# Performance work log

Measured on AMD Instinct MI355X. Metric: run time of the kernel, lower is better.

The kernel has to match this reference:

```python
import jax, jax.numpy as jnp
import numpy as np

B, S, D, H, M = 4, 4096, 768, 12, 256
Dh = D // H
EPS_KERNEL = 1e-4
LN_EPS = 1e-5


def setup_inputs() -> dict:
    key = jax.random.key(0)
    ks = jax.random.split(key, 18)
    w = lambda k, sh: jax.random.normal(k, sh, jnp.float32) * 0.02
    return {
        "x": jax.random.normal(ks[0], (B, S, D), jnp.float32),
        # FAVOR+ random projection (performer uses orthogonal gaussian; gaussian here, same math)
        "proj": jax.random.normal(ks[1], (M, Dh), jnp.float32),
        "wq": w(ks[2], (D, D)), "bq": jnp.zeros((D,), jnp.float32),
        "wk": w(ks[3], (D, D)), "bk": jnp.zeros((D,), jnp.float32),
        "wv": w(ks[4], (D, D)), "bv": jnp.zeros((D,), jnp.float32),
        "wo": w(ks[5], (D, D)), "bo": jnp.zeros((D,), jnp.float32),
        "ln1_g": jnp.ones((D,), jnp.float32), "ln1_b": jnp.zeros((D,), jnp.float32),
        "ln2_g": jnp.ones((D,), jnp.float32), "ln2_b": jnp.zeros((D,), jnp.float32),
        "w1": w(ks[6], (4 * D, D)), "b1": jnp.zeros((4 * D,), jnp.float32),
        "w2": w(ks[7], (D, 4 * D)), "b2": jnp.zeros((D,), jnp.float32),
    }


def layernorm(x, g, b):
    mu = x.mean(-1, keepdims=True)
    var = ((x - mu) ** 2).mean(-1, keepdims=True)
    return (x - mu) / jnp.sqrt(var + LN_EPS) * g + b


def softmax_features(data, proj, is_query):
    # FAVOR+ positive softmax kernel features (performer-pytorch softmax_kernel)
    norm = data.shape[-1] ** -0.25
    ratio = proj.shape[0] ** -0.5
    dd = jnp.einsum('bhnd,md->bhnm', data * norm, proj)       # [B,H,S,M]
    diag = (data ** 2).sum(-1, keepdims=True) * 0.5 * norm * norm
    if is_query:
        mx = jnp.max(dd, axis=-1, keepdims=True)
    else:
        mx = jnp.max(dd)
    return ratio * (jnp.exp(dd - diag - mx) + EPS_KERNEL)


def performer_block(x, proj, wq, bq, wk, bk, wv, bv, wo, bo,
                    ln1_g, ln1_b, ln2_g, ln2_b, w1, b1, w2, b2):
    h = layernorm(x, ln1_g, ln1_b)
    split = lambda t: t.reshape(B, S, H, Dh).transpose(0, 2, 1, 3)  # [B,H,S,Dh]
    q = split(h @ wq.T + bq)
    k = split(h @ wk.T + bk)
    v = split(h @ wv.T + bv)

    qp = softmax_features(q, proj, True)    # [B,H,S,M]
    kp = softmax_features(k, proj, False)   # [B,H,S,M]

    # non-causal linear attention
    k_sum = kp.sum(axis=2)                                   # [B,H,M]
    d_inv = 1.0 / jnp.einsum('bhnm,bhm->bhn', qp, k_sum)     # [B,H,S]
    ctx = jnp.einsum('bhnm,bhnd->bhmd', kp, v)               # [B,H,M,Dh]
    attn = jnp.einsum('bhnm,bhmd,bhn->bhnd', qp, ctx, d_inv) # [B,H,S,Dh]
    attn = attn.transpose(0, 2, 1, 3).reshape(B, S, D)
    x = x + attn @ wo.T + bo

    h2 = layernorm(x, ln2_g, ln2_b)
    h2 = jax.nn.gelu(h2 @ w1.T + b1, approximate=False)
    x = x + h2 @ w2.T + b2
    return x


def reference(x, proj, wq, bq, wk, bk, wv, bv, wo, bo,
              ln1_g, ln1_b, ln2_g, ln2_b, w1, b1, w2, b2):
    return performer_block(x, proj, wq, bq, wk, bk, wv, bv, wo, bo,
                           ln1_g, ln1_b, ln2_g, ln2_b, w1, b1, w2, b2)
```

## Files before the change

kernel.cpp:

```cpp
#include <hip/hip_runtime.h>
#include <math.h>

typedef __attribute__((ext_vector_type(8))) short bf16x8;
typedef __attribute__((ext_vector_type(4))) float f32x4;

__device__ __forceinline__ float b2f(unsigned short u) {
    return __uint_as_float(((unsigned)u) << 16);
}
__device__ __forceinline__ unsigned short f2b(float f) {
    unsigned u = __float_as_uint(f);
    u += 0x7FFF + ((u >> 16) & 1);
    return (unsigned short)(u >> 16);
}
__device__ __forceinline__ void up2(unsigned u, float& a, float& b) {
    a = __uint_as_float(u << 16);
    b = __uint_as_float(u & 0xffff0000u);
}
__device__ __forceinline__ float gelu_exact(float v) {
    return 0.5f * v * (1.0f + erff(v * 0.70710678118654752f));
}
__device__ __forceinline__ void atomicMaxFloat(float* addr, float val) {
    unsigned* ua = (unsigned*)addr;
    unsigned old = *ua;
    while (true) {
        float of = __uint_as_float(old);
        if (of >= val) break;
        unsigned assumed = old;
        old = atomicCAS(ua, assumed, __float_as_uint(val));
        if (old == assumed) break;
    }
}
__device__ __forceinline__ void gl_lds16(const unsigned short* g, unsigned short* lds) {
    __builtin_amdgcn_global_load_lds((const __attribute__((address_space(1))) unsigned int*)g,
                                     (__attribute__((address_space(3))) unsigned int*)lds, 16, 0, 0);
}

__global__ void init_kernel(float* ksum, float* kmax) {
    int i = blockIdx.x * 256 + threadIdx.x;
    if (i < 48 * 256) ksum[i] = 0.0f;
    if (i == 0) *kmax = -3.0e38f;
}

__global__ __launch_bounds__(256)
void cvt_qkvp(const float* __restrict__ wq, const float* __restrict__ wk, const float* __restrict__ wv,
              const float* __restrict__ prj, unsigned short* __restrict__ wdst,
              unsigned short* __restrict__ pdst) {
    int i4 = (blockIdx.x * 256 + threadIdx.x) * 4;
    const float* s; unsigned short* d; int off;
    if (i4 < 1769472) { s = (i4 < 589824) ? wq : (i4 < 1179648 ? wk : wv);
        off = (i4 < 589824) ? i4 : (i4 < 1179648 ? i4 - 589824 : i4 - 1179648);
        d = wdst + i4; }
    else { s = prj; off = i4 - 1769472; d = pdst + off; }
    float4 v = *(const float4*)&s[off];
    ushort4 o; o.x = f2b(v.x); o.y = f2b(v.y); o.z = f2b(v.z); o.w = f2b(v.w);
    *(ushort4*)d = o;
}
__global__ __launch_bounds__(256)
void cvt_ow12(const float* __restrict__ wo, const float* __restrict__ w1, const float* __restrict__ w2,
              unsigned short* __restrict__ dst) {
    int i4 = (blockIdx.x * 256 + threadIdx.x) * 4;
    const float* s; int off;
    if (i4 < 589824) { s = wo; off = i4; }
    else if (i4 < 2949120) { s = w1; off = i4 - 589824; }
    else { s = w2; off = i4 - 2949120; }
    float4 v = *(const float4*)&s[off];
    ushort4 o; o.x = f2b(v.x); o.y = f2b(v.y); o.z = f2b(v.z); o.w = f2b(v.w);
    *(ushort4*)&dst[i4] = o;
}

template <bool IN_F32>
__global__ __launch_bounds__(256)
void ln_kernel(const void* __restrict__ Xv, const float* __restrict__ G,
               const float* __restrict__ Bb, unsigned short* __restrict__ OUT) {
    int row = blockIdx.x, t = threadIdx.x, wave = t >> 6, lane = t & 63;
    __shared__ float red[4];
    float x0, x1, x2;
    if constexpr (IN_F32) {
        const float* xr = (const float*)Xv + (size_t)row * 768;
        x0 = xr[t]; x1 = xr[t + 256]; x2 = xr[t + 512];
    } else {
        const unsigned short* xr = (const unsigned short*)Xv + (size_t)row * 768;
        x0 = b2f(xr[t]); x1 = b2f(xr[t + 256]); x2 = b2f(xr[t + 512]);
    }
    float s = x0 + x1 + x2;
#pragma unroll
    for (int d = 32; d; d >>= 1) s += __shfl_xor(s, d, 64);
    if (lane == 0) red[wave] = s;
    __syncthreads();
    float mean = (red[0] + red[1] + red[2] + red[3]) * (1.0f / 768.0f);
    __syncthreads();
    float d0 = x0 - mean, d1 = x1 - mean, d2 = x2 - mean;
    float s2 = d0 * d0 + d1 * d1 + d2 * d2;
#pragma unroll
    for (int d = 32; d; d >>= 1) s2 += __shfl_xor(s2, d, 64);
    if (lane == 0) red[wave] = s2;
    __syncthreads();
    float var = (red[0] + red[1] + red[2] + red[3]) * (1.0f / 768.0f);
    float inv = rsqrtf(var + 1e-5f);
    size_t base = (size_t)row * 768;
    OUT[base + t]       = f2b(d0 * inv * G[t]       + Bb[t]);
    OUT[base + t + 256] = f2b(d1 * inv * G[t + 256] + Bb[t + 256]);
    OUT[base + t + 512] = f2b(d2 * inv * G[t + 512] + Bb[t + 512]);
}

template <int EPI, bool R_F32, bool C_F32>
__global__ __launch_bounds__(512)
void gemm_bt_256(const unsigned short* __restrict__ A, const unsigned short* __restrict__ Bm,
                 const float* __restrict__ bias, const void* __restrict__ R,
                 void* __restrict__ C, int N, int K, float alpha) {
    __shared__ unsigned short sA[2][256 * 32];
    __shared__ unsigned short sB[2][128 * 32];
    const int t = threadIdx.x;
    const int wave = t >> 6, lane = t & 63, quad = lane >> 4, l16 = lane & 15;
    const int nwg = gridDim.x * gridDim.y;
    int flat = blockIdx.y * gridDim.x + blockIdx.x;
    int q = nwg >> 3, r = nwg & 7;
    int xcd = flat & 7, idx = flat >> 3;
    int swz = (xcd < r ? xcd * (q + 1) : r * (q + 1) + (xcd - r) * q) + idx;
    const int m0 = (swz / gridDim.x) * 256;
    const int n0 = (swz % gridDim.x) * 128;
    const int wm = (wave >> 1) * 64, wn = (wave & 1) * 64;
    const int srow = t >> 2;
    const int scol = ((t & 3) ^ (srow & 3)) << 3;
    const unsigned short* ga0 = &A[(size_t)(m0 + srow) * K + scol];
    const unsigned short* ga1 = &A[(size_t)(m0 + 128 + srow) * K + scol];
    const unsigned short* gb  = &Bm[(size_t)(n0 + srow) * K + scol];
    const int ldsoff = wave * 512;
    const int sw = ((quad ^ l16) & 3) << 3;
    int raoff[4], rboff[4];
#pragma unroll
    for (int i = 0; i < 4; ++i) {
        raoff[i] = (wm + i * 16 + l16) * 32 + sw;
        rboff[i] = (wn + i * 16 + l16) * 32 + sw;
    }
    f32x4 acc[4][4] = {};
    const int nt = K >> 5;
    gl_lds16(ga0, &sA[0][ldsoff]);
    gl_lds16(ga1, &sA[0][4096 + ldsoff]);
    gl_lds16(gb,  &sB[0][ldsoff]);
    __syncthreads();
    int cur = 0;
    for (int it = 0; it < nt; ++it) {
        if (it + 1 < nt) {
            const int kt = (it + 1) << 5;
            gl_lds16(ga0 + kt, &sA[cur ^ 1][ldsoff]);
            gl_lds16(ga1 + kt, &sA[cur ^ 1][4096 + ldsoff]);
            gl_lds16(gb + kt,  &sB[cur ^ 1][ldsoff]);
        }
        bf16x8 af[4], bfr[4];
#pragma unroll
        for (int i = 0; i < 4; ++i) af[i] = *(const bf16x8*)&sA[cur][raoff[i]];
#pragma unroll
        for (int j = 0; j < 4; ++j) bfr[j] = *(const bf16x8*)&sB[cur][rboff[j]];
#pragma unroll
        for (int i = 0; i < 4; ++i)
#pragma unroll
            for (int j = 0; j < 4; ++j)
                acc[i][j] = __builtin_amdgcn_mfma_f32_16x16x32_bf16(af[i], bfr[j], acc[i][j], 0, 0, 0);
        __syncthreads();
        cur ^= 1;
    }
    if constexpr (EPI == 3) {
#pragma unroll
        for (int i = 0; i < 4; ++i) {
            int rowb = m0 + wm + i * 16 + quad * 4;
            int b_ = rowb >> 12, sbase = rowb & 4095;
#pragma unroll
            for (int j = 0; j < 4; ++j) {
                int col = n0 + wn + j * 16 + l16;
                float bs = bias[col];
                ushort4 o;
                o.x = f2b(acc[i][j][0] + bs);
                o.y = f2b(acc[i][j][1] + bs);
                o.z = f2b(acc[i][j][2] + bs);
                o.w = f2b(acc[i][j][3] + bs);
                size_t dst = (((size_t)b_ * 12 + (col >> 6)) * 64 + (col & 63)) * 4096 + sbase;
                *(ushort4*)&((unsigned short*)C)[dst] = o;
            }
        }
        return;
    }
#pragma unroll
    for (int i = 0; i < 4; ++i) {
        int rowb = m0 + wm + i * 16 + quad * 4;
#pragma unroll
        for (int j = 0; j < 4; ++j) {
            int col = n0 + wn + j * 16 + l16;
            float bs = bias[col];
#pragma unroll
            for (int r4 = 0; r4 < 4; ++r4) {
                size_t idx = (size_t)(rowb + r4) * N + col;
                float v = acc[i][j][r4] + bs;
                if constexpr (EPI == 0) v *= alpha;
                if constexpr (EPI == 1) {
                    if constexpr (R_F32) v += ((const float*)R)[idx];
                    else                 v += b2f(((const unsigned short*)R)[idx]);
                }
                if constexpr (EPI == 2) v = gelu_exact(v);
                if constexpr (C_F32) ((float*)C)[idx] = v;
                else                 ((unsigned short*)C)[idx] = f2b(v);
            }
        }
    }
}

template <int MODE>
__global__ __launch_bounds__(256)
void feat_kernel(const unsigned short* __restrict__ Q, const unsigned short* __restrict__ P,
                 unsigned short* __restrict__ OUTP, float* __restrict__ kmaxp,
                 float* __restrict__ ksump) {
    __shared__ unsigned short sQ[64 * 64];
    __shared__ unsigned short sP[256 * 64];
    __shared__ float sDiag[64];
    __shared__ float sRed[4];
    int t = threadIdx.x, wave = t >> 6, lane = t & 63, quad = lane >> 4, l16 = lane & 15;
    int bh = blockIdx.y, bq = bh / 12, hh = bh % 12;
    int s0 = blockIdx.x * 64;
    size_t rowbase = (size_t)bq * 4096 + s0;
#pragma unroll
    for (int u = 0; u < 2; ++u) {
        int L = u * 256 + t, row = L >> 3, c8 = (L & 7) * 8;
        *(uint4*)&sQ[row * 64 + c8] = *(const uint4*)&Q[(rowbase + row) * 768 + hh * 64 + c8];
    }
#pragma unroll
    for (int u = 0; u < 8; ++u) {
        int L = u * 256 + t, row = L >> 3, c8 = (L & 7) * 8;
        *(uint4*)&sP[row * 64 + c8] = *(const uint4*)&P[(size_t)row * 64 + c8];
    }
    __syncthreads();
    if (MODE != 1 && t < 64) {
        float d = 0.0f;
        for (int c = 0; c < 64; ++c) { float f = b2f(sQ[t * 64 + c]); d += f * f; }
        sDiag[t] = 0.5f * d;
    }
    f32x4 acc[4][4] = {};
#pragma unroll
    for (int ks = 0; ks < 2; ++ks) {
        bf16x8 af[4], bfr[4];
#pragma unroll
        for (int i = 0; i < 4; ++i) af[i] = *(const bf16x8*)&sQ[(i * 16 + l16) * 64 + ks * 32 + quad * 8];
#pragma unroll
        for (int j = 0; j < 4; ++j) bfr[j] = *(const bf16x8*)&sP[(wave * 64 + j * 16 + l16) * 64 + ks * 32 + quad * 8];
#pragma unroll
        for (int i = 0; i < 4; ++i)
#pragma unroll
            for (int j = 0; j < 4; ++j)
                acc[i][j] = __builtin_amdgcn_mfma_f32_16x16x32_bf16(af[i], bfr[j], acc[i][j], 0, 0, 0);
    }
    if constexpr (MODE == 1) {
        float m = -3.0e38f;
#pragma unroll
        for (int i = 0; i < 4; ++i)
#pragma unroll
            for (int j = 0; j < 4; ++j)
#pragma unroll
                for (int r = 0; r < 4; ++r) m = fmaxf(m, acc[i][j][r]);
#pragma unroll
        for (int d = 1; d < 64; d <<= 1) m = fmaxf(m, __shfl_xor(m, d, 64));
        if (lane == 0) sRed[wave] = m;
        __syncthreads();
        if (t == 0) atomicMaxFloat(kmaxp, fmaxf(fmaxf(sRed[0], sRed[1]), fmaxf(sRed[2], sRed[3])));
        return;
    } else {
        __syncthreads();
        float mx_k = *kmaxp;
        float csum[4] = {0.0f, 0.0f, 0.0f, 0.0f};
#pragma unroll
        for (int i = 0; i < 4; ++i)
#pragma unroll
            for (int j = 0; j < 4; ++j) {
                int col = wave * 64 + j * 16 + l16;
                ushort4 o;
#pragma unroll
                for (int r = 0; r < 4; ++r) {
                    int row = i * 16 + quad * 4 + r;
                    float v = 0.0625f * (expf(acc[i][j][r] - sDiag[row] - mx_k) + 1e-4f);
                    csum[j] += v;
                    (&o.x)[r] = f2b(v);
                }
                *(ushort4*)&OUTP[((size_t)bh * 256 + col) * 4096 + s0 + i * 16 + quad * 4] = o;
            }
#pragma unroll
        for (int j = 0; j < 4; ++j) {
            csum[j] += __shfl_xor(csum[j], 16, 64);
            csum[j] += __shfl_xor(csum[j], 32, 64);
        }
        if (quad == 0)
#pragma unroll
            for (int j = 0; j < 4; ++j)
                atomicAdd(&ksump[bh * 256 + wave * 64 + j * 16 + l16], csum[j]);
    }
}

__global__ __launch_bounds__(256)
void ctx_gemm(const unsigned short* __restrict__ KPT, const unsigned short* __restrict__ VT,
              float* __restrict__ part) {
    __shared__ unsigned short sV[2][64 * 32];
    __shared__ unsigned short sK[2][128 * 32];
    const int t = threadIdx.x;
    const int wave = t >> 6, lane = t & 63, quad = lane >> 4, l16 = lane & 15;
    const int bh = blockIdx.y;
    const int sc = blockIdx.x >> 1, mh = blockIdx.x & 1;
    const int m0 = mh * 128;
    const int k0 = sc * 512;
    const int srow = t >> 2;
    const int scol = ((t & 3) ^ (srow & 3)) << 3;
    const unsigned short* gv  = &VT [((size_t)bh * 64 + srow) * 4096 + k0 + scol];
    const unsigned short* gk0 = &KPT[((size_t)bh * 256 + m0 + srow) * 4096 + k0 + scol];
    const unsigned short* gk1 = &KPT[((size_t)bh * 256 + m0 + 64 + srow) * 4096 + k0 + scol];
    const int ldsoff = wave * 512;
    const int sw = ((quad ^ l16) & 3) << 3;
    f32x4 acc[4][2] = {};
    gl_lds16(gv,  &sV[0][ldsoff]);
    gl_lds16(gk0, &sK[0][ldsoff]);
    gl_lds16(gk1, &sK[0][2048 + ldsoff]);
    __syncthreads();
    int cur = 0;
    for (int it = 0; it < 16; ++it) {
        if (it + 1 < 16) {
            const int kt = (it + 1) << 5;
            gl_lds16(gv + kt,  &sV[cur ^ 1][ldsoff]);
            gl_lds16(gk0 + kt, &sK[cur ^ 1][ldsoff]);
            gl_lds16(gk1 + kt, &sK[cur ^ 1][2048 + ldsoff]);
        }
        bf16x8 af[4], bfr[2];
#pragma unroll
        for (int i = 0; i < 4; ++i) af[i] = *(const bf16x8*)&sV[cur][(i * 16 + l16) * 32 + sw];
#pragma unroll
        for (int j = 0; j < 2; ++j) bfr[j] = *(const bf16x8*)&sK[cur][(wave * 32 + j * 16 + l16) * 32 + sw];
#pragma unroll
        for (int i = 0; i < 4; ++i)
#pragma unroll
            for (int j = 0; j < 2; ++j)
                acc[i][j] = __builtin_amdgcn_mfma_f32_16x16x32_bf16(af[i], bfr[j], acc[i][j], 0, 0, 0);
        __syncthreads();
        cur ^= 1;
    }
    float* base = part + ((size_t)(sc * 48 + bh) * 64) * 256;
#pragma unroll
    for (int i = 0; i < 4; ++i)
#pragma unroll
        for (int r = 0; r < 4; ++r) {
            int d = i * 16 + quad * 4 + r;
#pragma unroll
            for (int j = 0; j < 2; ++j) {
                int m = m0 + wave * 32 + j * 16 + l16;
                base[(size_t)d * 256 + m] = acc[i][j][r];
            }
        }
}

__global__ __launch_bounds__(256)
void ctx_reduce(const float* __restrict__ part, unsigned short* __restrict__ ctxb) {
    size_t i = (size_t)blockIdx.x * 256 + threadIdx.x;
    float s = 0.0f;
#pragma unroll
    for (int c = 0; c < 8; ++c) s += part[(size_t)c * 786432 + i];
    ctxb[i] = f2b(s);
}

__global__ __launch_bounds__(256)
void feat_attn(const unsigned short* __restrict__ Q, const unsigned short* __restrict__ P,
               const unsigned short* __restrict__ CTX, const float* __restrict__ ksump,
               unsigned short* __restrict__ ATT) {
    __shared__ unsigned short sQ[64 * 64];
    __shared__ unsigned short sPQ[256 * 64];
    __shared__ unsigned short sCtx[64 * 256];
    __shared__ float sDiag[64];
    __shared__ float sRed[256];
    __shared__ float sWred[256];
    __shared__ float sKs[256];
    __shared__ float sDinv[64];
    int t = threadIdx.x, wave = t >> 6, lane = t & 63, quad = lane >> 4, l16 = lane & 15;
    int bh = blockIdx.y, bq = bh / 12, hh = bh % 12;
    int s0 = blockIdx.x * 64;
    size_t rowbase = (size_t)bq * 4096 + s0;
#pragma unroll
    for (int u = 0; u < 2; ++u) {
        int L = u * 256 + t, row = L >> 3, c8 = (L & 7) * 8;
        *(uint4*)&sQ[row * 64 + c8] = *(const uint4*)&Q[(rowbase + row) * 768 + hh * 64 + c8];
    }
#pragma unroll
    for (int u = 0; u < 8; ++u) {
        int L = u * 256 + t, row = L >> 3, c8 = (L & 7) * 8;
        *(uint4*)&sPQ[row * 64 + c8] = *(const uint4*)&P[(size_t)row * 64 + c8];
    }
#pragma unroll
    for (int u = 0; u < 8; ++u) {
        int L = u * 256 + t, d = L >> 5, m8 = L & 31;
        int m8s = (m8 & 28) | ((m8 ^ d) & 3);
        *(uint4*)&sCtx[d * 256 + m8s * 8] = *(const uint4*)&CTX[(size_t)bh * 16384 + d * 256 + m8 * 8];
    }
    sKs[t] = ksump[bh * 256 + t];
    __syncthreads();
    if (t < 64) {
        float d = 0.0f;
        for (int c = 0; c < 64; ++c) { float f = b2f(sQ[t * 64 + c]); d += f * f; }
        sDiag[t] = 0.5f * d;
    }
    f32x4 acc[4][4] = {};
#pragma unroll
    for (int ks = 0; ks < 2; ++ks) {
        bf16x8 af[4], bfr[4];
#pragma unroll
        for (int i = 0; i < 4; ++i) af[i] = *(const bf16x8*)&sQ[(i * 16 + l16) * 64 + ks * 32 + quad * 8];
#pragma unroll
        for (int j = 0; j < 4; ++j) bfr[j] = *(const bf16x8*)&sPQ[(wave * 64 + j * 16 + l16) * 64 + ks * 32 + quad * 8];
#pragma unroll
        for (int i = 0; i < 4; ++i)
#pragma unroll
            for (int j = 0; j < 4; ++j)
                acc[i][j] = __builtin_amdgcn_mfma_f32_16x16x32_bf16(af[i], bfr[j], acc[i][j], 0, 0, 0);
    }
#pragma unroll
    for (int i = 0; i < 4; ++i)
#pragma unroll
        for (int r = 0; r < 4; ++r) {
            float m = fmaxf(fmaxf(acc[i][0][r], acc[i][1][r]), fmaxf(acc[i][2][r], acc[i][3][r]));
#pragma unroll
            for (int d = 1; d < 16; d <<= 1) m = fmaxf(m, __shfl_xor(m, d, 64));
            if (l16 == 0) sRed[wave * 64 + i * 16 + quad * 4 + r] = m;
        }
    __syncthreads();
    if (t < 64) sRed[t] = fmaxf(fmaxf(sRed[t], sRed[64 + t]), fmaxf(sRed[128 + t], sRed[192 + t]));
    __syncthreads();
#pragma unroll
    for (int i = 0; i < 4; ++i)
#pragma unroll
        for (int r = 0; r < 4; ++r) {
            int row = i * 16 + quad * 4 + r;
            float diag = sDiag[row], mx = sRed[row];
            float p = 0.0f;
#pragma unroll
            for (int j = 0; j < 4; ++j) {
                int col = wave * 64 + j * 16 + l16;
                float v = 0.0625f * (expf(acc[i][j][r] - diag - mx) + 1e-4f);
                int colp = (col & ~31) | ((((col >> 3) ^ row) & 3) << 3) | (col & 7);
                sPQ[row * 256 + colp] = f2b(v);
                p += v * sKs[col];
            }
#pragma unroll
            for (int d = 1; d < 16; d <<= 1) p += __shfl_xor(p, d, 64);
            if (l16 == 0) sWred[wave * 64 + row] = p;
        }
    __syncthreads();
    if (t < 64) sDinv[t] = 1.0f / (sWred[t] + sWred[64 + t] + sWred[128 + t] + sWred[192 + t]);
    __syncthreads();
    const int w16 = wave * 16;
    const int aswz = ((quad ^ (l16 & 3)) << 3);
    f32x4 acc2[4] = {};
    const unsigned short* qrow = &sPQ[(w16 + l16) * 256];
#pragma unroll
    for (int kt = 0; kt < 256; kt += 32) {
        bf16x8 af = *(const bf16x8*)&qrow[kt + aswz];
#pragma unroll
        for (int j = 0; j < 4; ++j) {
            bf16x8 bf = *(const bf16x8*)&sCtx[(j * 16 + l16) * 256 + kt + aswz];
            acc2[j] = __builtin_amdgcn_mfma_f32_16x16x32_bf16(af, bf, acc2[j], 0, 0, 0);
        }
    }
#pragma unroll
    for (int rr = 0; rr < 4; ++rr) {
        int sr = w16 + quad * 4 + rr;
        float dv = sDinv[sr];
        size_t obase = ((size_t)bq * 4096 + s0 + sr) * 768 + hh * 64;
#pragma unroll
        for (int j = 0; j < 4; ++j)
            ATT[obase + j * 16 + l16] = f2b(acc2[j][rr] * dv);
    }
}

extern "C" void kernel_launch(void* const* d_in, const int* in_sizes, int n_in,
                              void* d_out, int out_size, void* d_ws, size_t ws_size,
                              hipStream_t stream) {
    const float* X   = (const float*)d_in[0];
    const float* PRJ = (const float*)d_in[1];
    const float* WQ  = (const float*)d_in[2];
    const float* BQ  = (const float*)d_in[3];
    const float* WK  = (const float*)d_in[4];
    const float* BKb = (const float*)d_in[5];
    const float* WV  = (const float*)d_in[6];
    const float* BV  = (const float*)d_in[7];
    const float* WO  = (const float*)d_in[8];
    const float* BO  = (const float*)d_in[9];
    const float* G1  = (const float*)d_in[10];
    const float* Bn1 = (const float*)d_in[11];
    const float* G2  = (const float*)d_in[12];
    const float* Bn2 = (const float*)d_in[13];
    const float* W1  = (const float*)d_in[14];
    const float* Bf1 = (const float*)d_in[15];
    const float* W2  = (const float*)d_in[16];
    const float* Bf2 = (const float*)d_in[17];
    float* OUT = (float*)d_out;

    char* w = (char*)d_ws;
    const size_t SZ_ACT = (size_t)16384 * 768 * 2;
    unsigned short* hbuf  = (unsigned short*)(w);
    float*          part  = (float*)(w);
    unsigned short* qn    = (unsigned short*)(w + SZ_ACT);
    unsigned short* wow12 = (unsigned short*)(w + SZ_ACT);
    unsigned short* kn    = (unsigned short*)(w + 2 * SZ_ACT);
    unsigned short* x2    = (unsigned short*)(w + 2 * SZ_ACT);
    unsigned short* vtb   = (unsigned short*)(w + 3 * SZ_ACT);
    unsigned short* attn  = (unsigned short*)(w + 3 * SZ_ACT);
    unsigned short* wqkv  = (unsigned short*)(w + 4 * SZ_ACT);
    unsigned short* kpt   = (unsigned short*)(w + 4 * SZ_ACT);
    unsigned short* gmid  = kpt;
    char* tail = w + 4 * SZ_ACT + (size_t)100663296;
    unsigned short* prjb = (unsigned short*)(tail);
    unsigned short* ctxb = (unsigned short*)(tail + 32768);
    float* ksum = (float*)(tail + 32768 + 1572864);
    float* kmax = (float*)(tail + 32768 + 1572864 + 49152);

    unsigned short* wqb = wqkv;
    unsigned short* wkb = wqkv + 589824;
    unsigned short* wvb = wqkv + 1179648;
    unsigned short* wob = wow12;
    unsigned short* w1b = wow12 + 589824;
    unsigned short* w2b = wow12 + 2949120;

    const float NORM = 0.35355339059327373f;

    init_kernel<<<48, 256, 0, stream>>>(ksum, kmax);
    cvt_qkvp<<<1744, 256, 0, stream>>>(WQ, WK, WV, PRJ, wqkv, prjb);
    ln_kernel<true><<<16384, 256, 0, stream>>>(X, G1, Bn1, hbuf);
    gemm_bt_256<0, false, false><<<dim3(6, 64), 512, 0, stream>>>(hbuf, wqb, BQ, nullptr, qn, 768, 768, NORM);
    gemm_bt_256<0, false, false><<<dim3(6, 64), 512, 0, stream>>>(hbuf, wkb, BKb, nullptr, kn, 768, 768, NORM);
    gemm_bt_256<3, false, false><<<dim3(6, 64), 512, 0, stream>>>(hbuf, wvb, BV, nullptr, vtb, 768, 768, 1.0f);
    feat_kernel<1><<<dim3(64, 48), 256, 0, stream>>>(kn, prjb, nullptr, kmax, ksum);
    feat_kernel<2><<<dim3(64, 48), 256, 0, stream>>>(kn, prjb, kpt, kmax, ksum);
    ctx_gemm<<<dim3(16, 48), 256, 0, stream>>>(kpt, vtb, part);
    ctx_reduce<<<3072, 256, 0, stream>>>(part, ctxb);
    feat_attn<<<dim3(64, 48), 256, 0, stream>>>(qn, prjb, ctxb, ksum, attn);
    cvt_ow12<<<5184, 256, 0, stream>>>(WO, W1, W2, wow12);
    gemm_bt_256<1, true, false><<<dim3(6, 64), 512, 0, stream>>>(attn, wob, BO, X, x2, 768, 768, 1.0f);
    ln_kernel<false><<<16384, 256, 0, stream>>>(x2, G2, Bn2, hbuf);
    gemm_bt_256<2, false, false><<<dim3(24, 64), 512, 0, stream>>>(hbuf, w1b, Bf1, nullptr, gmid, 3072, 768, 1.0f);
    gemm_bt_256<1, false, true><<<dim3(6, 64), 512, 0, stream>>>(gmid, w2b, Bf2, x2, OUT, 768, 3072, 1.0f);
}
```

Before: 811.8 us.

## Enlarge GEMM tiles to 256x256 with 64-deep K steps

The bf16 MFMA GEMM moves from 256x128 tiles with K-step 32 to 256x256 tiles with K-step 64. Each wave now computes a 128x64 sub-tile, and the LDS swizzle is widened to 8 chunks. This raises arithmetic intensity and halves the number of K iterations and barriers. In exchange LDS use grows to 128KB per block, register pressure doubles, and the grid halves (192 blocks for the 768-wide GEMMs), which may underfill the 256 CUs.

```diff
diff --git a/kernel.cpp b/kernel.cpp
--- a/kernel.cpp
+++ b/kernel.cpp
@@ -104,12 +104,12 @@
 }
 
 template <int EPI, bool R_F32, bool C_F32>
-__global__ __launch_bounds__(512)
+__global__ __launch_bounds__(512, 2)
 void gemm_bt_256(const unsigned short* __restrict__ A, const unsigned short* __restrict__ Bm,
                  const float* __restrict__ bias, const void* __restrict__ R,
                  void* __restrict__ C, int N, int K, float alpha) {
-    __shared__ unsigned short sA[2][256 * 32];
-    __shared__ unsigned short sB[2][128 * 32];
+    __shared__ unsigned short sA[2][256 * 64];
+    __shared__ unsigned short sB[2][256 * 64];
     const int t = threadIdx.x;
     const int wave = t >> 6, lane = t & 63, quad = lane >> 4, l16 = lane & 15;
     const int nwg = gridDim.x * gridDim.y;
@@ -118,51 +118,62 @@
     int xcd = flat & 7, idx = flat >> 3;
     int swz = (xcd < r ? xcd * (q + 1) : r * (q + 1) + (xcd - r) * q) + idx;
     const int m0 = (swz / gridDim.x) * 256;
-    const int n0 = (swz % gridDim.x) * 128;
-    const int wm = (wave >> 1) * 64, wn = (wave & 1) * 64;
-    const int srow = t >> 2;
-    const int scol = ((t & 3) ^ (srow & 3)) << 3;
-    const unsigned short* ga0 = &A[(size_t)(m0 + srow) * K + scol];
-    const unsigned short* ga1 = &A[(size_t)(m0 + 128 + srow) * K + scol];
-    const unsigned short* gb  = &Bm[(size_t)(n0 + srow) * K + scol];
-    const int ldsoff = wave * 512;
-    const int sw = ((quad ^ l16) & 3) << 3;
-    int raoff[4], rboff[4];
-#pragma unroll
-    for (int i = 0; i < 4; ++i) {
-        raoff[i] = (wm + i * 16 + l16) * 32 + sw;
-        rboff[i] = (wn + i * 16 + l16) * 32 + sw;
-    }
-    f32x4 acc[4][4] = {};
-    const int nt = K >> 5;
-    gl_lds16(ga0, &sA[0][ldsoff]);
-    gl_lds16(ga1, &sA[0][4096 + ldsoff]);
-    gl_lds16(gb,  &sB[0][ldsoff]);
+    const int n0 = (swz % gridDim.x) * 256;
+    const int wm = (wave >> 2) * 128, wn = (wave & 3) * 64;
+    const int srow = t >> 3;
+    const int scol = ((t & 7) ^ (srow & 7)) << 3;
+    const unsigned short* gA = &A[(size_t)(m0 + srow) * K + scol];
+    const unsigned short* gB = &Bm[(size_t)(n0 + srow) * K + scol];
+    const size_t rstep = (size_t)64 * K;
+    unsigned short* ldA0 = &sA[0][wave * 512];
+    unsigned short* ldB0 = &sB[0][wave * 512];
+    unsigned short* ldA1 = &sA[1][wave * 512];
+    unsigned short* ldB1 = &sB[1][wave * 512];
+    const int k0off = ((quad ^ (l16 & 7)) & 7) << 3;
+    const int k1off = (((4 | quad) ^ (l16 & 7)) & 7) << 3;
+    f32x4 acc[8][4] = {};
+    const int nt = K >> 6;
+#pragma unroll
+    for (int u = 0; u < 4; ++u) {
+        gl_lds16(gA + u * rstep, ldA0 + u * 4096);
+        gl_lds16(gB + u * rstep, ldB0 + u * 4096);
+    }
     __syncthreads();
     int cur = 0;
     for (int it = 0; it < nt; ++it) {
         if (it + 1 < nt) {
-            const int kt = (it + 1) << 5;
-            gl_lds16(ga0 + kt, &sA[cur ^ 1][ldsoff]);
-            gl_lds16(ga1 + kt, &sA[cur ^ 1][4096 + ldsoff]);
-            gl_lds16(gb + kt,  &sB[cur ^ 1][ldsoff]);
-        }
-        bf16x8 af[4], bfr[4];
-#pragma unroll
-        for (int i = 0; i < 4; ++i) af[i] = *(const bf16x8*)&sA[cur][raoff[i]];
-#pragma unroll
-        for (int j = 0; j < 4; ++j) bfr[j] = *(const bf16x8*)&sB[cur][rboff[j]];
-#pragma unroll
-        for (int i = 0; i < 4; ++i)
+            const size_t kt = (size_t)(it + 1) << 6;
+            unsigned short* dA = cur ? ldA0 : ldA1;
+            unsigned short* dB = cur ? ldB0 : ldB1;
+#pragma unroll
+            for (int u = 0; u < 4; ++u) {
+                gl_lds16(gA + u * rstep + kt, dA + u * 4096);
+                gl_lds16(gB + u * rstep + kt, dB + u * 4096);
+            }
+        }
+        const unsigned short* bufA = cur ? &sA[1][0] : &sA[0][0];
+        const unsigned short* bufB = cur ? &sB[1][0] : &sB[0][0];
+#pragma unroll
+        for (int ks = 0; ks < 2; ++ks) {
+            const int koff = ks ? k1off : k0off;
+            bf16x8 bfr[4];
 #pragma unroll
             for (int j = 0; j < 4; ++j)
-                acc[i][j] = __builtin_amdgcn_mfma_f32_16x16x32_bf16(af[i], bfr[j], acc[i][j], 0, 0, 0);
+                bfr[j] = *(const bf16x8*)&bufB[(wn + j * 16 + l16) * 64 + koff];
+#pragma unroll
+            for (int i = 0; i < 8; ++i) {
+                bf16x8 af = *(const bf16x8*)&bufA[(wm + i * 16 + l16) * 64 + koff];
+#pragma unroll
+                for (int j = 0; j < 4; ++j)
+                    acc[i][j] = __builtin_amdgcn_mfma_f32_16x16x32_bf16(af, bfr[j], acc[i][j], 0, 0, 0);
+            }
+        }
         __syncthreads();
         cur ^= 1;
     }
     if constexpr (EPI == 3) {
 #pragma unroll
-        for (int i = 0; i < 4; ++i) {
+        for (int i = 0; i < 8; ++i) {
             int rowb = m0 + wm + i * 16 + quad * 4;
             int b_ = rowb >> 12, sbase = rowb & 4095;
 #pragma unroll
@@ -181,7 +192,7 @@
         return;
     }
 #pragma unroll
-    for (int i = 0; i < 4; ++i) {
+    for (int i = 0; i < 8; ++i) {
         int rowb = m0 + wm + i * 16 + quad * 4;
 #pragma unroll
         for (int j = 0; j < 4; ++j) {
@@ -524,17 +535,17 @@
     init_kernel<<<48, 256, 0, stream>>>(ksum, kmax);
     cvt_qkvp<<<1744, 256, 0, stream>>>(WQ, WK, WV, PRJ, wqkv, prjb);
     ln_kernel<true><<<16384, 256, 0, stream>>>(X, G1, Bn1, hbuf);
-    gemm_bt_256<0, false, false><<<dim3(6, 64), 512, 0, stream>>>(hbuf, wqb, BQ, nullptr, qn, 768, 768, NORM);
-    gemm_bt_256<0, false, false><<<dim3(6, 64), 512, 0, stream>>>(hbuf, wkb, BKb, nullptr, kn, 768, 768, NORM);
-    gemm_bt_256<3, false, false><<<dim3(6, 64), 512, 0, stream>>>(hbuf, wvb, BV, nullptr, vtb, 768, 768, 1.0f);
+    gemm_bt_256<0, false, false><<<dim3(3, 64), 512, 0, stream>>>(hbuf, wqb, BQ, nullptr, qn, 768, 768, NORM);
+    gemm_bt_256<0, false, false><<<dim3(3, 64), 512, 0, stream>>>(hbuf, wkb, BKb, nullptr, kn, 768, 768, NORM);
+    gemm_bt_256<3, false, false><<<dim3(3, 64), 512, 0, stream>>>(hbuf, wvb, BV, nullptr, vtb, 768, 768, 1.0f);
     feat_kernel<1><<<dim3(64, 48), 256, 0, stream>>>(kn, prjb, nullptr, kmax, ksum);
     feat_kernel<2><<<dim3(64, 48), 256, 0, stream>>>(kn, prjb, kpt, kmax, ksum);
     ctx_gemm<<<dim3(16, 48), 256, 0, stream>>>(kpt, vtb, part);
     ctx_reduce<<<3072, 256, 0, stream>>>(part, ctxb);
     feat_attn<<<dim3(64, 48), 256, 0, stream>>>(qn, prjb, ctxb, ksum, attn);
     cvt_ow12<<<5184, 256, 0, stream>>>(WO, W1, W2, wow12);
-    gemm_bt_256<1, true, false><<<dim3(6, 64), 512, 0, stream>>>(attn, wob, BO, X, x2, 768, 768, 1.0f);
+    gemm_bt_256<1, true, false><<<dim3(3, 64), 512, 0, stream>>>(attn, wob, BO, X, x2, 768, 768, 1.0f);
     ln_kernel<false><<<16384, 256, 0, stream>>>(x2, G2, Bn2, hbuf);
-    gemm_bt_256<2, false, false><<<dim3(24, 64), 512, 0, stream>>>(hbuf, w1b, Bf1, nullptr, gmid, 3072, 768, 1.0f);
-    gemm_bt_256<1, false, true><<<dim3(6, 64), 512, 0, stream>>>(gmid, w2b, Bf2, x2, OUT, 768, 3072, 1.0f);
-}
+    gemm_bt_256<2, false, false><<<dim3(12, 64), 512, 0, stream>>>(hbuf, w1b, Bf1, nullptr, gmid, 3072, 768, 1.0f);
+    gemm_bt_256<1, false, true><<<dim3(3, 64), 512, 0, stream>>>(gmid, w2b, Bf2, x2, OUT, 768, 3072, 1.0f);
+}
```

Result: faster. 684.1 us (-15.7%).

## Deepen GEMM pipeline to four LDS stages with explicit vmcnt waits and wider tiles

Applied to the files above, without the earlier changes.

Rewrites the shared bf16 GEMM to prefetch four K-tiles ahead into a 4-slot LDS ring, using explicit s_waitcnt vmcnt counts and raw s_barrier instead of __syncthreads. Waves are rearranged into a 2x4 grid, each computing 128 rows, and the FFN1 GEMM gets 256-wide N tiles. The changes also add setprio around the MFMA block and a launch-bounds occupancy hint of 2. The aim is to hide global-load latency and raise MFMA density. In exchange it uses more LDS and accumulator registers per wave, which can lower occupancy or cause spills.

```diff
diff --git a/kernel.cpp b/kernel.cpp
--- a/kernel.cpp
+++ b/kernel.cpp
@@ -33,6 +33,15 @@
 __device__ __forceinline__ void gl_lds16(const unsigned short* g, unsigned short* lds) {
     __builtin_amdgcn_global_load_lds((const __attribute__((address_space(1))) unsigned int*)g,
                                      (__attribute__((address_space(3))) unsigned int*)lds, 16, 0, 0);
+}
+template <int N> __device__ __forceinline__ void wait_vm() {
+    if constexpr (N == 0)  asm volatile("s_waitcnt vmcnt(0)" ::: "memory");
+    if constexpr (N == 3)  asm volatile("s_waitcnt vmcnt(3)" ::: "memory");
+    if constexpr (N == 4)  asm volatile("s_waitcnt vmcnt(4)" ::: "memory");
+    if constexpr (N == 6)  asm volatile("s_waitcnt vmcnt(6)" ::: "memory");
+    if constexpr (N == 8)  asm volatile("s_waitcnt vmcnt(8)" ::: "memory");
+    if constexpr (N == 9)  asm volatile("s_waitcnt vmcnt(9)" ::: "memory");
+    if constexpr (N == 12) asm volatile("s_waitcnt vmcnt(12)" ::: "memory");
 }
 
 __global__ void init_kernel(float* ksum, float* kmax) {
@@ -103,13 +112,15 @@
     OUT[base + t + 512] = f2b(d2 * inv * G[t + 512] + Bb[t + 512]);
 }
 
-template <int EPI, bool R_F32, bool C_F32>
-__global__ __launch_bounds__(512)
+template <int EPI, bool R_F32, bool C_F32, int BN>
+__global__ __launch_bounds__(512, 2)
 void gemm_bt_256(const unsigned short* __restrict__ A, const unsigned short* __restrict__ Bm,
                  const float* __restrict__ bias, const void* __restrict__ R,
                  void* __restrict__ C, int N, int K, float alpha) {
-    __shared__ unsigned short sA[2][256 * 32];
-    __shared__ unsigned short sB[2][128 * 32];
+    constexpr int NJ = BN / 64;
+    constexpr int LPT = 2 + BN / 128;
+    __shared__ unsigned short sA[4][8192];
+    __shared__ unsigned short sB[4][BN * 32];
     const int t = threadIdx.x;
     const int wave = t >> 6, lane = t & 63, quad = lane >> 4, l16 = lane & 15;
     const int nwg = gridDim.x * gridDim.y;
@@ -118,55 +129,66 @@
     int xcd = flat & 7, idx = flat >> 3;
     int swz = (xcd < r ? xcd * (q + 1) : r * (q + 1) + (xcd - r) * q) + idx;
     const int m0 = (swz / gridDim.x) * 256;
-    const int n0 = (swz % gridDim.x) * 128;
-    const int wm = (wave >> 1) * 64, wn = (wave & 1) * 64;
-    const int srow = t >> 2;
-    const int scol = ((t & 3) ^ (srow & 3)) << 3;
-    const unsigned short* ga0 = &A[(size_t)(m0 + srow) * K + scol];
-    const unsigned short* ga1 = &A[(size_t)(m0 + 128 + srow) * K + scol];
-    const unsigned short* gb  = &Bm[(size_t)(n0 + srow) * K + scol];
-    const int ldsoff = wave * 512;
-    const int sw = ((quad ^ l16) & 3) << 3;
-    int raoff[4], rboff[4];
-#pragma unroll
-    for (int i = 0; i < 4; ++i) {
-        raoff[i] = (wm + i * 16 + l16) * 32 + sw;
-        rboff[i] = (wn + i * 16 + l16) * 32 + sw;
-    }
-    f32x4 acc[4][4] = {};
+    const int n0 = (swz % gridDim.x) * BN;
+    const int wm = (wave >> 2) * 128;
+    const int wn = (wave & 3) * (BN / 4);
+    const int srowc = t >> 2;
+    const int scol = ((t & 3) ^ ((t >> 3) & 3)) << 3;
+    const unsigned short* gA0 = &A[(size_t)(m0 + srowc) * K + scol];
+    const unsigned short* gA1 = &A[(size_t)(m0 + 128 + srowc) * K + scol];
+    const unsigned short* gB0 = &Bm[(size_t)(n0 + srowc) * K + scol];
+    const unsigned short* gB1 = (BN == 256) ? &Bm[(size_t)(n0 + 128 + srowc) * K + scol] : gB0;
+    const int koff = ((quad ^ ((l16 >> 1) & 3)) & 3) << 3;
+    f32x4 acc[8][NJ] = {};
     const int nt = K >> 5;
-    gl_lds16(ga0, &sA[0][ldsoff]);
-    gl_lds16(ga1, &sA[0][4096 + ldsoff]);
-    gl_lds16(gb,  &sB[0][ldsoff]);
-    __syncthreads();
-    int cur = 0;
+    auto STAGE = [&](int tile, int slot) {
+        const size_t kt = (size_t)tile << 5;
+        unsigned short* dA = &sA[slot][wave * 512];
+        unsigned short* dB = &sB[slot][wave * 512];
+        gl_lds16(gA0 + kt, dA);
+        gl_lds16(gA1 + kt, dA + 4096);
+        gl_lds16(gB0 + kt, dB);
+        if constexpr (BN == 256) gl_lds16(gB1 + kt, dB + 4096);
+    };
+    STAGE(0, 0); STAGE(1, 1); STAGE(2, 2); STAGE(3, 3);
     for (int it = 0; it < nt; ++it) {
-        if (it + 1 < nt) {
-            const int kt = (it + 1) << 5;
-            gl_lds16(ga0 + kt, &sA[cur ^ 1][ldsoff]);
-            gl_lds16(ga1 + kt, &sA[cur ^ 1][4096 + ldsoff]);
-            gl_lds16(gb + kt,  &sB[cur ^ 1][ldsoff]);
-        }
-        bf16x8 af[4], bfr[4];
-#pragma unroll
-        for (int i = 0; i < 4; ++i) af[i] = *(const bf16x8*)&sA[cur][raoff[i]];
-#pragma unroll
-        for (int j = 0; j < 4; ++j) bfr[j] = *(const bf16x8*)&sB[cur][rboff[j]];
-#pragma unroll
-        for (int i = 0; i < 4; ++i)
-#pragma unroll
-            for (int j = 0; j < 4; ++j)
-                acc[i][j] = __builtin_amdgcn_mfma_f32_16x16x32_bf16(af[i], bfr[j], acc[i][j], 0, 0, 0);
-        __syncthreads();
-        cur ^= 1;
+        const int slot = it & 3;
+        const int rem = nt - 1 - it;
+        if (rem >= 3)      wait_vm<3 * LPT>();
+        else if (rem == 2) wait_vm<2 * LPT>();
+        else if (rem == 1) wait_vm<1 * LPT>();
+        else               wait_vm<0>();
+        __builtin_amdgcn_s_barrier();
+        __builtin_amdgcn_sched_barrier(0);
+        {
+            const unsigned short* bA = sA[slot];
+            const unsigned short* bB = sB[slot];
+            bf16x8 bfr[NJ];
+#pragma unroll
+            for (int j = 0; j < NJ; ++j)
+                bfr[j] = *(const bf16x8*)&bB[(wn + j * 16 + l16) * 32 + koff];
+            __builtin_amdgcn_s_setprio(1);
+#pragma unroll
+            for (int i = 0; i < 8; ++i) {
+                bf16x8 af = *(const bf16x8*)&bA[(wm + i * 16 + l16) * 32 + koff];
+#pragma unroll
+                for (int j = 0; j < NJ; ++j)
+                    acc[i][j] = __builtin_amdgcn_mfma_f32_16x16x32_bf16(af, bfr[j], acc[i][j], 0, 0, 0);
+            }
+            __builtin_amdgcn_s_setprio(0);
+        }
+        __builtin_amdgcn_sched_barrier(0);
+        __builtin_amdgcn_s_barrier();
+        __builtin_amdgcn_sched_barrier(0);
+        if (it + 4 < nt) STAGE(it + 4, slot);
     }
     if constexpr (EPI == 3) {
 #pragma unroll
-        for (int i = 0; i < 4; ++i) {
+        for (int i = 0; i < 8; ++i) {
             int rowb = m0 + wm + i * 16 + quad * 4;
             int b_ = rowb >> 12, sbase = rowb & 4095;
 #pragma unroll
-            for (int j = 0; j < 4; ++j) {
+            for (int j = 0; j < NJ; ++j) {
                 int col = n0 + wn + j * 16 + l16;
                 float bs = bias[col];
                 ushort4 o;
@@ -181,10 +203,10 @@
         return;
     }
 #pragma unroll
-    for (int i = 0; i < 4; ++i) {
+    for (int i = 0; i < 8; ++i) {
         int rowb = m0 + wm + i * 16 + quad * 4;
 #pragma unroll
-        for (int j = 0; j < 4; ++j) {
+        for (int j = 0; j < NJ; ++j) {
             int col = n0 + wn + j * 16 + l16;
             float bs = bias[col];
 #pragma unroll
@@ -524,17 +546,17 @@
     init_kernel<<<48, 256, 0, stream>>>(ksum, kmax);
     cvt_qkvp<<<1744, 256, 0, stream>>>(WQ, WK, WV, PRJ, wqkv, prjb);
     ln_kernel<true><<<16384, 256, 0, stream>>>(X, G1, Bn1, hbuf);
-    gemm_bt_256<0, false, false><<<dim3(6, 64), 512, 0, stream>>>(hbuf, wqb, BQ, nullptr, qn, 768, 768, NORM);
-    gemm_bt_256<0, false, false><<<dim3(6, 64), 512, 0, stream>>>(hbuf, wkb, BKb, nullptr, kn, 768, 768, NORM);
-    gemm_bt_256<3, false, false><<<dim3(6, 64), 512, 0, stream>>>(hbuf, wvb, BV, nullptr, vtb, 768, 768, 1.0f);
+    gemm_bt_256<0, false, false, 128><<<dim3(6, 64), 512, 0, stream>>>(hbuf, wqb, BQ, nullptr, qn, 768, 768, NORM);
+    gemm_bt_256<0, false, false, 128><<<dim3(6, 64), 512, 0, stream>>>(hbuf, wkb, BKb, nullptr, kn, 768, 768, NORM);
+    gemm_bt_256<3, false, false, 128><<<dim3(6, 64), 512, 0, stream>>>(hbuf, wvb, BV, nullptr, vtb, 768, 768, 1.0f);
     feat_kernel<1><<<dim3(64, 48), 256, 0, stream>>>(kn, prjb, nullptr, kmax, ksum);
     feat_kernel<2><<<dim3(64, 48), 256, 0, stream>>>(kn, prjb, kpt, kmax, ksum);
     ctx_gemm<<<dim3(16, 48), 256, 0, stream>>>(kpt, vtb, part);
     ctx_reduce<<<3072, 256, 0, stream>>>(part, ctxb);
     feat_attn<<<dim3(64, 48), 256, 0, stream>>>(qn, prjb, ctxb, ksum, attn);
     cvt_ow12<<<5184, 256, 0, stream>>>(WO, W1, W2, wow12);
-    gemm_bt_256<1, true, false><<<dim3(6, 64), 512, 0, stream>>>(attn, wob, BO, X, x2, 768, 768, 1.0f);
+    gemm_bt_256<1, true, false, 128><<<dim3(6, 64), 512, 0, stream>>>(attn, wob, BO, X, x2, 768, 768, 1.0f);
     ln_kernel<false><<<16384, 256, 0, stream>>>(x2, G2, Bn2, hbuf);
-    gemm_bt_256<2, false, false><<<dim3(24, 64), 512, 0, stream>>>(hbuf, w1b, Bf1, nullptr, gmid, 3072, 768, 1.0f);
-    gemm_bt_256<1, false, true><<<dim3(6, 64), 512, 0, stream>>>(gmid, w2b, Bf2, x2, OUT, 768, 3072, 1.0f);
-}
+    gemm_bt_256<2, false, false, 256><<<dim3(12, 64), 512, 0, stream>>>(hbuf, w1b, Bf1, nullptr, gmid, 3072, 768, 1.0f);
+    gemm_bt_256<1, false, true, 128><<<dim3(6, 64), 512, 0, stream>>>(gmid, w2b, Bf2, x2, OUT, 768, 3072, 1.0f);
+}
```

Result: slower. 871.1 us (+7.3%).
